# Performance work log

Measured on AMD Instinct MI355X. Metric: run time of the kernel, lower is better.

Reference implementation:

```python
import jax, jax.numpy as jnp
import numpy as np

# irreps: 256x0e + 128x1o + 64x2e  -> feature dim 256 + 384 + 320 = 960
M0, M1, M2 = 256, 128, 64
LOG2 = float(np.log(2.0))

# e3nn normalize2mom constant for shifted-softplus: 1/sqrt(E_{z~N(0,1)}[ssp(z)^2])
_z = np.linspace(-10.0, 10.0, 200001)
_phi = np.exp(-0.5 * _z ** 2) / np.sqrt(2.0 * np.pi)
_f = np.logaddexp(0.0, _z) - LOG2
C_SSP = float(1.0 / np.sqrt(np.trapz(_f ** 2 * _phi, _z)))


def _ssp(x):
    # shifted softplus, normalized to unit second moment as in e3nn Activation
    return C_SSP * (jax.nn.softplus(x) - LOG2)


def setup_inputs() -> dict:
    key = jax.random.key(0)
    ks = jax.random.split(key, 7)
    n = 65536
    return {
        "x": jax.random.normal(ks[0], (n, M0 + 3 * M1 + 5 * M2), dtype=jnp.float32),
        # linear1: l=0 block maps 256x0e -> (256 scalars + 192 gates)x0e
        "w1_s": jax.random.normal(ks[1], (M0, M0 + M1 + M2), dtype=jnp.float32),
        "w1_v1": jax.random.normal(ks[2], (M1, M1), dtype=jnp.float32),
        "w1_v2": jax.random.normal(ks[3], (M2, M2), dtype=jnp.float32),
        # linear2: gate.irreps_out -> irreps_in
        "w2_s": jax.random.normal(ks[4], (M0, M0), dtype=jnp.float32),
        "w2_v1": jax.random.normal(ks[5], (M1, M1), dtype=jnp.float32),
        "w2_v2": jax.random.normal(ks[6], (M2, M2), dtype=jnp.float32),
    }


def reference(x, w1_s, w1_v1, w1_v2, w2_s, w2_v1, w2_v2):
    n = x.shape[0]
    # split input into irrep segments
    x0 = x[:, :M0]                                  # [n, 256] scalars (0e)
    x1 = x[:, M0:M0 + 3 * M1].reshape(n, M1, 3)     # [n, 128, 3] (1o)
    x2 = x[:, M0 + 3 * M1:].reshape(n, M2, 5)       # [n, 64, 5]  (2e)

    # linear1 (per-l block matmuls, e3nn 1/sqrt(fan_in) normalization, no bias)
    s = (x0 @ w1_s) * (1.0 / np.sqrt(M0))                   # [n, 448]
    v1 = jnp.einsum('nic,io->noc', x1, w1_v1) * (1.0 / np.sqrt(M1))
    v2 = jnp.einsum('nic,io->noc', x2, w1_v2) * (1.0 / np.sqrt(M2))

    # Gate: activate scalars, activate gates, multiply gated irreps by gates
    scalars = _ssp(s[:, :M0])          # [n, 256]
    gates = _ssp(s[:, M0:])            # [n, 192] = 128 (for 1o) + 64 (for 2e)
    v1 = v1 * gates[:, :M1, None]
    v2 = v2 * gates[:, M1:, None]

    # linear2
    y0 = (scalars @ w2_s) * (1.0 / np.sqrt(M0))
    y1 = jnp.einsum('nic,io->noc', v1, w2_v1) * (1.0 / np.sqrt(M1))
    y2 = jnp.einsum('nic,io->noc', v2, w2_v2) * (1.0 / np.sqrt(M2))

    y = jnp.concatenate([y0, y1.reshape(n, -1), y2.reshape(n, -1)], axis=1)
    return x + y  # resnet
```

## Files before the change

kernel.cpp:

```cpp
#include <hip/hip_runtime.h>
#include <math.h>

#define XP 960
typedef __attribute__((ext_vector_type(8))) short short8;
typedef __attribute__((ext_vector_type(4))) float f32x4;
typedef __attribute__((ext_vector_type(4))) float fv4;
typedef __attribute__((ext_vector_type(4))) unsigned uint4v;

__device__ short g_pack[221184];

__device__ __forceinline__ short f2bf(float f) {
    union { float f; unsigned u; } v; v.f = f;
    unsigned r = (v.u + 0x7fffu + ((v.u >> 16) & 1u)) >> 16;
    return (short)r;
}
__device__ __forceinline__ unsigned pk2(float a, float b) {
    union { float f; unsigned u; } x, y; x.f = a; y.f = b;
    return ((x.u + 0x8000u) >> 16) | ((y.u + 0x8000u) & 0xffff0000u);
}
__device__ __forceinline__ short8 mk8(unsigned d0, unsigned d1, unsigned d2, unsigned d3) {
    union { uint4v u; short8 s; } cv;
    cv.u = (uint4v){d0, d1, d2, d3};
    return cv.s;
}
__device__ __forceinline__ float ssp(float v, float c) {
    float t = exp2f(fabsf(v) * -1.44269504088896340736f);
    float sp = fmaxf(v, 0.f) + 0.69314718055994530942f * __log2f(1.0f + t);
    return c * (sp - 0.69314718055994530942f);
}

#define WSYNC() asm volatile("s_waitcnt lgkmcnt(0)" ::: "memory")
#define MFMA(a, b, c) __builtin_amdgcn_mfma_f32_16x16x32_bf16((a), (b), (c), 0, 0, 0)
#define NTL(p) __builtin_nontemporal_load((const fv4*)(p))
#define STS(p, v) (*(fv4*)(p) = (v))

__global__ void pack_weights(const float* __restrict__ w1s, const float* __restrict__ w1v1,
                             const float* __restrict__ w1v2, const float* __restrict__ w2s,
                             const float* __restrict__ w2v1, const float* __restrict__ w2v2) {
    int g = blockIdx.x * blockDim.x + threadIdx.x;
    const float* src; int NT, N, dstoff, lg;
    if      (g < 14336) { src = w1s;  NT = 28; N = 448; dstoff = 0;      lg = g; }
    else if (g < 16384) { src = w1v1; NT = 8;  N = 128; dstoff = 114688; lg = g - 14336; }
    else if (g < 16896) { src = w1v2; NT = 4;  N = 64;  dstoff = 131072; lg = g - 16384; }
    else if (g < 25088) { src = w2s;  NT = 16; N = 256; dstoff = 135168; lg = g - 16896; }
    else if (g < 27136) { src = w2v1; NT = 8;  N = 128; dstoff = 200704; lg = g - 25088; }
    else if (g < 27648) { src = w2v2; NT = 4;  N = 64;  dstoff = 217088; lg = g - 27136; }
    else return;
    int lane = lg & 63;
    int t = lg >> 6;
    int nt = t % NT;
    int kt = t / NT;
    int k0 = kt * 32 + (lane >> 4) * 8;
    int n  = nt * 16 + (lane & 15);
    short* dst = g_pack + dstoff + (size_t)lg * 8;
#pragma unroll
    for (int j = 0; j < 8; j++) dst[j] = f2bf(src[(size_t)(k0 + j) * N + n]);
}

__global__ __launch_bounds__(256, 4) void fused_kernel(const float* __restrict__ x,
                                                       float* __restrict__ out,
                                                       float c_ssp) {
    __shared__ __align__(16) short arena[4][16 * 264];

    const int lane = threadIdx.x & 63;
    const int wave = threadIdx.x >> 6;
    const int q = lane >> 4, l15 = lane & 15;
    const int row0 = blockIdx.x * 64 + wave * 16;
    short* S = arena[wave];
    unsigned* Sd = (unsigned*)S;
    const int dwb = l15 * 132 + q * 2;
    const short* Sr = S + l15 * 264 + q * 8;

    const short8* pw1s  = (const short8*)(g_pack + 0);
    const short8* pw1v1 = (const short8*)(g_pack + 114688);
    const short8* pw1v2 = (const short8*)(g_pack + 131072);
    const short8* pw2s  = (const short8*)(g_pack + 135168);
    const short8* pw2v1 = (const short8*)(g_pack + 200704);
    const short8* pw2v2 = (const short8*)(g_pack + 217088);

    const float* xrow = x + (size_t)(row0 + l15) * XP;
    float* yrow = out + (size_t)(row0 + l15) * XP;

    const float S1  = 0.0625f;
    const float SV1 = 0.08838834764831845f;
    const float SV2 = 0.125f;

    short8 xf0[8];
#pragma unroll
    for (int kt = 0; kt < 8; kt++) {
        fv4 u0 = *(const fv4*)(xrow + kt * 32 + q * 8);
        fv4 u1 = *(const fv4*)(xrow + kt * 32 + q * 8 + 4);
        xf0[kt] = mk8(pk2(u0[0], u0[1]), pk2(u0[2], u0[3]), pk2(u1[0], u1[1]), pk2(u1[2], u1[3]));
    }

#pragma unroll 1
    for (int tp = 0; tp < 8; tp++) {
        f32x4 a0 = {0.f,0.f,0.f,0.f}, a1 = {0.f,0.f,0.f,0.f};
#pragma unroll
        for (int kt = 0; kt < 8; kt++) {
            a0 = MFMA(pw1s[(kt * 28 + 2 * tp + 0) * 64 + lane], xf0[kt], a0);
            a1 = MFMA(pw1s[(kt * 28 + 2 * tp + 1) * 64 + lane], xf0[kt], a1);
        }
#pragma unroll
        for (int h = 0; h < 2; h++) {
            f32x4 a = h ? a1 : a0;
            int t = 2 * tp + h;
            Sd[dwb + t * 8]     = pk2(ssp(a[0] * S1, c_ssp), ssp(a[1] * S1, c_ssp));
            Sd[dwb + t * 8 + 1] = pk2(ssp(a[2] * S1, c_ssp), ssp(a[3] * S1, c_ssp));
        }
    }
    f32x4 gacc[12];
#pragma unroll
    for (int tp = 0; tp < 6; tp++) {
        f32x4 a0 = {0.f,0.f,0.f,0.f}, a1 = {0.f,0.f,0.f,0.f};
#pragma unroll
        for (int kt = 0; kt < 8; kt++) {
            a0 = MFMA(pw1s[(kt * 28 + 16 + 2 * tp + 0) * 64 + lane], xf0[kt], a0);
            a1 = MFMA(pw1s[(kt * 28 + 16 + 2 * tp + 1) * 64 + lane], xf0[kt], a1);
        }
        gacc[2 * tp]     = (f32x4){ssp(a0[0]*S1,c_ssp), ssp(a0[1]*S1,c_ssp), ssp(a0[2]*S1,c_ssp), ssp(a0[3]*S1,c_ssp)};
        gacc[2 * tp + 1] = (f32x4){ssp(a1[0]*S1,c_ssp), ssp(a1[1]*S1,c_ssp), ssp(a1[2]*S1,c_ssp), ssp(a1[3]*S1,c_ssp)};
    }
    WSYNC();

    short8 sf[8];
#pragma unroll
    for (int kt = 0; kt < 8; kt++) sf[kt] = *(const short8*)(Sr + kt * 32);
    WSYNC();
#pragma unroll 1
    for (int tp = 0; tp < 8; tp++) {
        f32x4 a0 = {0.f,0.f,0.f,0.f}, a1 = {0.f,0.f,0.f,0.f};
#pragma unroll
        for (int kt = 0; kt < 8; kt++) {
            a0 = MFMA(pw2s[(kt * 16 + 2 * tp + 0) * 64 + lane], sf[kt], a0);
            a1 = MFMA(pw2s[(kt * 16 + 2 * tp + 1) * 64 + lane], sf[kt], a1);
        }
#pragma unroll
        for (int h = 0; h < 2; h++) {
            f32x4 a = h ? a1 : a0;
            int col = (2 * tp + h) * 16 + q * 4;
            fv4 r = NTL(xrow + col);
            fv4 o = {r[0] + a[0] * S1, r[1] + a[1] * S1, r[2] + a[2] * S1, r[3] + a[3] * S1};
            STS(yrow + col, o);
        }
    }

    short8 xf1[3][4];
#pragma unroll
    for (int kt = 0; kt < 4; kt++) {
        float b[24];
        const float* p = xrow + 256 + 3 * (kt * 32 + q * 8);
#pragma unroll
        for (int i = 0; i < 6; i++) *(fv4*)(b + 4 * i) = *(const fv4*)(p + 4 * i);
#pragma unroll
        for (int c = 0; c < 3; c++)
            xf1[c][kt] = mk8(pk2(b[c], b[c+3]), pk2(b[c+6], b[c+9]),
                             pk2(b[c+12], b[c+15]), pk2(b[c+18], b[c+21]));
    }
    short8 vf[3][4];
#pragma unroll
    for (int c = 0; c < 3; c++) {
#pragma unroll
        for (int tp = 0; tp < 4; tp++) {
            f32x4 a0 = {0.f,0.f,0.f,0.f}, a1 = {0.f,0.f,0.f,0.f};
#pragma unroll
            for (int kt = 0; kt < 4; kt++) {
                a0 = MFMA(pw1v1[(kt * 8 + 2 * tp + 0) * 64 + lane], xf1[c][kt], a0);
                a1 = MFMA(pw1v1[(kt * 8 + 2 * tp + 1) * 64 + lane], xf1[c][kt], a1);
            }
#pragma unroll
            for (int h = 0; h < 2; h++) {
                f32x4 a = h ? a1 : a0;
                int t = 2 * tp + h;
                f32x4 g = gacc[t];
                Sd[dwb + t * 8]     = pk2(a[0]*SV1*g[0], a[1]*SV1*g[1]);
                Sd[dwb + t * 8 + 1] = pk2(a[2]*SV1*g[2], a[3]*SV1*g[3]);
            }
        }
        WSYNC();
#pragma unroll
        for (int kt = 0; kt < 4; kt++)
            vf[c][kt] = *(const short8*)(Sr + kt * 32);
        WSYNC();
    }
#pragma unroll 1
    for (int t = 0; t < 8; t++) {
        f32x4 ac0 = {0.f,0.f,0.f,0.f}, ac1 = {0.f,0.f,0.f,0.f}, ac2 = {0.f,0.f,0.f,0.f};
#pragma unroll
        for (int kt = 0; kt < 4; kt++) {
            short8 w = pw2v1[(kt * 8 + t) * 64 + lane];
            ac0 = MFMA(w, vf[0][kt], ac0);
            ac1 = MFMA(w, vf[1][kt], ac1);
            ac2 = MFMA(w, vf[2][kt], ac2);
        }
        int base = 256 + 3 * (t * 16 + q * 4);
        fv4 r0 = NTL(xrow + base), r1 = NTL(xrow + base + 4), r2 = NTL(xrow + base + 8);
        fv4 o0 = {r0[0]+ac0[0]*SV1, r0[1]+ac1[0]*SV1, r0[2]+ac2[0]*SV1, r0[3]+ac0[1]*SV1};
        fv4 o1 = {r1[0]+ac1[1]*SV1, r1[1]+ac2[1]*SV1, r1[2]+ac0[2]*SV1, r1[3]+ac1[2]*SV1};
        fv4 o2 = {r2[0]+ac2[2]*SV1, r2[1]+ac0[3]*SV1, r2[2]+ac1[3]*SV1, r2[3]+ac2[3]*SV1};
        STS(yrow + base, o0); STS(yrow + base + 4, o1); STS(yrow + base + 8, o2);
    }

    short8 xf2[5][2];
#pragma unroll
    for (int kt = 0; kt < 2; kt++) {
        float b[40];
        const float* p = xrow + 640 + 5 * (kt * 32 + q * 8);
#pragma unroll
        for (int i = 0; i < 10; i++) *(fv4*)(b + 4 * i) = *(const fv4*)(p + 4 * i);
#pragma unroll
        for (int c = 0; c < 5; c++)
            xf2[c][kt] = mk8(pk2(b[c], b[c+5]), pk2(b[c+10], b[c+15]),
                             pk2(b[c+20], b[c+25]), pk2(b[c+30], b[c+35]));
    }
    short8 vf2[5][2];
#pragma unroll
    for (int c = 0; c < 5; c++) {
#pragma unroll
        for (int tp = 0; tp < 2; tp++) {
            f32x4 a0 = {0.f,0.f,0.f,0.f}, a1 = {0.f,0.f,0.f,0.f};
#pragma unroll
            for (int kt = 0; kt < 2; kt++) {
                a0 = MFMA(pw1v2[(kt * 4 + 2 * tp + 0) * 64 + lane], xf2[c][kt], a0);
                a1 = MFMA(pw1v2[(kt * 4 + 2 * tp + 1) * 64 + lane], xf2[c][kt], a1);
            }
#pragma unroll
            for (int h = 0; h < 2; h++) {
                f32x4 a = h ? a1 : a0;
                int t = 2 * tp + h;
                f32x4 g = gacc[8 + t];
                Sd[dwb + t * 8]     = pk2(a[0]*SV2*g[0], a[1]*SV2*g[1]);
                Sd[dwb + t * 8 + 1] = pk2(a[2]*SV2*g[2], a[3]*SV2*g[3]);
            }
        }
        WSYNC();
#pragma unroll
        for (int kt = 0; kt < 2; kt++)
            vf2[c][kt] = *(const short8*)(Sr + kt * 32);
        WSYNC();
    }
#pragma unroll 1
    for (int t = 0; t < 4; t++) {
        f32x4 b0 = {0.f,0.f,0.f,0.f}, b1 = {0.f,0.f,0.f,0.f}, b2 = {0.f,0.f,0.f,0.f},
              b3 = {0.f,0.f,0.f,0.f}, b4 = {0.f,0.f,0.f,0.f};
#pragma unroll
        for (int kt = 0; kt < 2; kt++) {
            short8 w = pw2v2[(kt * 4 + t) * 64 + lane];
            b0 = MFMA(w, vf2[0][kt], b0);
            b1 = MFMA(w, vf2[1][kt], b1);
            b2 = MFMA(w, vf2[2][kt], b2);
            b3 = MFMA(w, vf2[3][kt], b3);
            b4 = MFMA(w, vf2[4][kt], b4);
        }
        int base = 640 + 5 * (t * 16 + q * 4);
        fv4 r0 = NTL(xrow + base),      r1 = NTL(xrow + base + 4),
            r2 = NTL(xrow + base + 8),  r3 = NTL(xrow + base + 12),
            r4 = NTL(xrow + base + 16);
        fv4 o0 = {r0[0]+b0[0]*SV2, r0[1]+b1[0]*SV2, r0[2]+b2[0]*SV2, r0[3]+b3[0]*SV2};
        fv4 o1 = {r1[0]+b4[0]*SV2, r1[1]+b0[1]*SV2, r1[2]+b1[1]*SV2, r1[3]+b2[1]*SV2};
        fv4 o2 = {r2[0]+b3[1]*SV2, r2[1]+b4[1]*SV2, r2[2]+b0[2]*SV2, r2[3]+b1[2]*SV2};
        fv4 o3 = {r3[0]+b2[2]*SV2, r3[1]+b3[2]*SV2, r3[2]+b4[2]*SV2, r3[3]+b0[3]*SV2};
        fv4 o4 = {r4[0]+b1[3]*SV2, r4[1]+b2[3]*SV2, r4[2]+b3[3]*SV2, r4[3]+b4[3]*SV2};
        STS(yrow + base, o0); STS(yrow + base + 4, o1); STS(yrow + base + 8, o2);
        STS(yrow + base + 12, o3); STS(yrow + base + 16, o4);
    }
}

static float compute_cssp() {
    const int N = 200001;
    const double dz = 20.0 / 200000.0;
    double sum = 0.0;
    for (int i = 0; i < N; i++) {
        double z = -10.0 + dz * i;
        double f = (z > 0 ? z : 0.0) + log1p(exp(-fabs(z))) - 0.69314718055994530942;
        double phi = exp(-0.5 * z * z) * 0.39894228040143267794;
        double y = f * f * phi;
        sum += (i == 0 || i == N - 1) ? 0.5 * y : y;
    }
    return (float)(1.0 / sqrt(sum * dz));
}

extern "C" void kernel_launch(void* const* d_in, const int* in_sizes, int n_in,
                              void* d_out, int out_size, void* d_ws, size_t ws_size,
                              hipStream_t stream) {
    const float* x    = (const float*)d_in[0];
    const float* w1s  = (const float*)d_in[1];
    const float* w1v1 = (const float*)d_in[2];
    const float* w1v2 = (const float*)d_in[3];
    const float* w2s  = (const float*)d_in[4];
    const float* w2v1 = (const float*)d_in[5];
    const float* w2v2 = (const float*)d_in[6];
    float* out = (float*)d_out;

    static const float c_ssp = compute_cssp();

    int rows = in_sizes[0] / XP;
    int blocks = rows / 64;

    pack_weights<<<108, 256, 0, stream>>>(w1s, w1v1, w1v2, w2s, w2v1, w2v2);
    fused_kernel<<<blocks, 256, 0, stream>>>(x, out, c_ssp);
}
```

Baseline: 631.8 us.

## Process two 16-row tiles per wave to reuse weight fragments across MFMAs

Each wave now handles 32 rows (two 16-row tiles A and B), so every weight fragment loaded from global memory feeds two MFMAs, halving weight traffic per row. The LDS staging buffer is resized to an unpadded 256-wide layout with an XOR swizzle to avoid bank conflicts. Gate activations are kept packed as bf16 pairs to save registers. Launch bounds drop to 2 blocks per CU and the grid halves, which increases register pressure and reduces occupancy and latency hiding.

```diff
diff --git a/kernel.cpp b/kernel.cpp
--- a/kernel.cpp
+++ b/kernel.cpp
@@ -22,6 +22,12 @@
     union { uint4v u; short8 s; } cv;
     cv.u = (uint4v){d0, d1, d2, d3};
     return cv.s;
+}
+__device__ __forceinline__ float bflo(unsigned d) {
+    union { unsigned u; float f; } v; v.u = d << 16; return v.f;
+}
+__device__ __forceinline__ float bfhi(unsigned d) {
+    union { unsigned u; float f; } v; v.u = d & 0xffff0000u; return v.f;
 }
 __device__ __forceinline__ float ssp(float v, float c) {
     float t = exp2f(fabsf(v) * -1.44269504088896340736f);
@@ -57,19 +63,24 @@
     for (int j = 0; j < 8; j++) dst[j] = f2bf(src[(size_t)(k0 + j) * N + n]);
 }
 
-__global__ __launch_bounds__(256, 4) void fused_kernel(const float* __restrict__ x,
+__global__ __launch_bounds__(256, 2) void fused_kernel(const float* __restrict__ x,
                                                        float* __restrict__ out,
                                                        float c_ssp) {
-    __shared__ __align__(16) short arena[4][16 * 264];
+    __shared__ __align__(16) short arena[4][32 * 256];
 
     const int lane = threadIdx.x & 63;
     const int wave = threadIdx.x >> 6;
     const int q = lane >> 4, l15 = lane & 15;
-    const int row0 = blockIdx.x * 64 + wave * 16;
+    const int row0 = blockIdx.x * 128 + wave * 32;
     short* S = arena[wave];
     unsigned* Sd = (unsigned*)S;
-    const int dwb = l15 * 132 + q * 2;
-    const short* Sr = S + l15 * 264 + q * 8;
+
+    const unsigned swzd = (unsigned)((l15 & 7) << 2);
+    const int wlinA = l15 * 128 + q * 2;
+    const int wlinB = wlinA + 2048;
+    const int rlinA = l15 * 512 + q * 16;
+    const int rlinB = rlinA + 8192;
+#define LDSR(linbyte) (*(const short8*)((const char*)S + (((unsigned)(linbyte)) ^ (swzd << 2))))
 
     const short8* pw1s  = (const short8*)(g_pack + 0);
     const short8* pw1v1 = (const short8*)(g_pack + 114688);
@@ -78,192 +89,297 @@
     const short8* pw2v1 = (const short8*)(g_pack + 200704);
     const short8* pw2v2 = (const short8*)(g_pack + 217088);
 
-    const float* xrow = x + (size_t)(row0 + l15) * XP;
-    float* yrow = out + (size_t)(row0 + l15) * XP;
+    const float* xrowA = x + (size_t)(row0 + l15) * XP;
+    const float* xrowB = xrowA + (size_t)16 * XP;
+    float* yrowA = out + (size_t)(row0 + l15) * XP;
+    float* yrowB = yrowA + (size_t)16 * XP;
 
     const float S1  = 0.0625f;
     const float SV1 = 0.08838834764831845f;
     const float SV2 = 0.125f;
 
-    short8 xf0[8];
+    short8 xfA[8], xfB[8];
 #pragma unroll
     for (int kt = 0; kt < 8; kt++) {
-        fv4 u0 = *(const fv4*)(xrow + kt * 32 + q * 8);
-        fv4 u1 = *(const fv4*)(xrow + kt * 32 + q * 8 + 4);
-        xf0[kt] = mk8(pk2(u0[0], u0[1]), pk2(u0[2], u0[3]), pk2(u1[0], u1[1]), pk2(u1[2], u1[3]));
+        fv4 a0 = *(const fv4*)(xrowA + kt * 32 + q * 8);
+        fv4 a1 = *(const fv4*)(xrowA + kt * 32 + q * 8 + 4);
+        fv4 b0 = *(const fv4*)(xrowB + kt * 32 + q * 8);
+        fv4 b1 = *(const fv4*)(xrowB + kt * 32 + q * 8 + 4);
+        xfA[kt] = mk8(pk2(a0[0], a0[1]), pk2(a0[2], a0[3]), pk2(a1[0], a1[1]), pk2(a1[2], a1[3]));
+        xfB[kt] = mk8(pk2(b0[0], b0[1]), pk2(b0[2], b0[3]), pk2(b1[0], b1[1]), pk2(b1[2], b1[3]));
     }
 
 #pragma unroll 1
     for (int tp = 0; tp < 8; tp++) {
-        f32x4 a0 = {0.f,0.f,0.f,0.f}, a1 = {0.f,0.f,0.f,0.f};
+        f32x4 a0A = {0.f,0.f,0.f,0.f}, a1A = {0.f,0.f,0.f,0.f};
+        f32x4 a0B = {0.f,0.f,0.f,0.f}, a1B = {0.f,0.f,0.f,0.f};
 #pragma unroll
         for (int kt = 0; kt < 8; kt++) {
-            a0 = MFMA(pw1s[(kt * 28 + 2 * tp + 0) * 64 + lane], xf0[kt], a0);
-            a1 = MFMA(pw1s[(kt * 28 + 2 * tp + 1) * 64 + lane], xf0[kt], a1);
+            short8 w0 = pw1s[(kt * 28 + 2 * tp + 0) * 64 + lane];
+            short8 w1 = pw1s[(kt * 28 + 2 * tp + 1) * 64 + lane];
+            a0A = MFMA(w0, xfA[kt], a0A);
+            a0B = MFMA(w0, xfB[kt], a0B);
+            a1A = MFMA(w1, xfA[kt], a1A);
+            a1B = MFMA(w1, xfB[kt], a1B);
         }
 #pragma unroll
         for (int h = 0; h < 2; h++) {
-            f32x4 a = h ? a1 : a0;
+            f32x4 aA = h ? a1A : a0A, aB = h ? a1B : a0B;
             int t = 2 * tp + h;
-            Sd[dwb + t * 8]     = pk2(ssp(a[0] * S1, c_ssp), ssp(a[1] * S1, c_ssp));
-            Sd[dwb + t * 8 + 1] = pk2(ssp(a[2] * S1, c_ssp), ssp(a[3] * S1, c_ssp));
-        }
-    }
-    f32x4 gacc[12];
+            { unsigned i = ((unsigned)(wlinA + t * 8)) ^ swzd;
+              Sd[i]     = pk2(ssp(aA[0] * S1, c_ssp), ssp(aA[1] * S1, c_ssp));
+              Sd[i + 1] = pk2(ssp(aA[2] * S1, c_ssp), ssp(aA[3] * S1, c_ssp)); }
+            { unsigned i = ((unsigned)(wlinB + t * 8)) ^ swzd;
+              Sd[i]     = pk2(ssp(aB[0] * S1, c_ssp), ssp(aB[1] * S1, c_ssp));
+              Sd[i + 1] = pk2(ssp(aB[2] * S1, c_ssp), ssp(aB[3] * S1, c_ssp)); }
+        }
+    }
+    unsigned gpkA[24], gpkB[24];
 #pragma unroll
     for (int tp = 0; tp < 6; tp++) {
-        f32x4 a0 = {0.f,0.f,0.f,0.f}, a1 = {0.f,0.f,0.f,0.f};
+        f32x4 a0A = {0.f,0.f,0.f,0.f}, a1A = {0.f,0.f,0.f,0.f};
+        f32x4 a0B = {0.f,0.f,0.f,0.f}, a1B = {0.f,0.f,0.f,0.f};
 #pragma unroll
         for (int kt = 0; kt < 8; kt++) {
-            a0 = MFMA(pw1s[(kt * 28 + 16 + 2 * tp + 0) * 64 + lane], xf0[kt], a0);
-            a1 = MFMA(pw1s[(kt * 28 + 16 + 2 * tp + 1) * 64 + lane], xf0[kt], a1);
-        }
-        gacc[2 * tp]     = (f32x4){ssp(a0[0]*S1,c_ssp), ssp(a0[1]*S1,c_ssp), ssp(a0[2]*S1,c_ssp), ssp(a0[3]*S1,c_ssp)};
-        gacc[2 * tp + 1] = (f32x4){ssp(a1[0]*S1,c_ssp), ssp(a1[1]*S1,c_ssp), ssp(a1[2]*S1,c_ssp), ssp(a1[3]*S1,c_ssp)};
+            short8 w0 = pw1s[(kt * 28 + 16 + 2 * tp + 0) * 64 + lane];
+            short8 w1 = pw1s[(kt * 28 + 16 + 2 * tp + 1) * 64 + lane];
+            a0A = MFMA(w0, xfA[kt], a0A);
+            a0B = MFMA(w0, xfB[kt], a0B);
+            a1A = MFMA(w1, xfA[kt], a1A);
+            a1B = MFMA(w1, xfB[kt], a1B);
+        }
+        gpkA[4*tp+0] = pk2(ssp(a0A[0]*S1,c_ssp), ssp(a0A[1]*S1,c_ssp));
+        gpkA[4*tp+1] = pk2(ssp(a0A[2]*S1,c_ssp), ssp(a0A[3]*S1,c_ssp));
+        gpkA[4*tp+2] = pk2(ssp(a1A[0]*S1,c_ssp), ssp(a1A[1]*S1,c_ssp));
+        gpkA[4*tp+3] = pk2(ssp(a1A[2]*S1,c_ssp), ssp(a1A[3]*S1,c_ssp));
+        gpkB[4*tp+0] = pk2(ssp(a0B[0]*S1,c_ssp), ssp(a0B[1]*S1,c_ssp));
+        gpkB[4*tp+1] = pk2(ssp(a0B[2]*S1,c_ssp), ssp(a0B[3]*S1,c_ssp));
+        gpkB[4*tp+2] = pk2(ssp(a1B[0]*S1,c_ssp), ssp(a1B[1]*S1,c_ssp));
+        gpkB[4*tp+3] = pk2(ssp(a1B[2]*S1,c_ssp), ssp(a1B[3]*S1,c_ssp));
     }
     WSYNC();
 
-    short8 sf[8];
-#pragma unroll
-    for (int kt = 0; kt < 8; kt++) sf[kt] = *(const short8*)(Sr + kt * 32);
+    short8 sfA[8], sfB[8];
+#pragma unroll
+    for (int kt = 0; kt < 8; kt++) {
+        sfA[kt] = LDSR(rlinA + kt * 64);
+        sfB[kt] = LDSR(rlinB + kt * 64);
+    }
     WSYNC();
 #pragma unroll 1
     for (int tp = 0; tp < 8; tp++) {
-        f32x4 a0 = {0.f,0.f,0.f,0.f}, a1 = {0.f,0.f,0.f,0.f};
+        f32x4 a0A = {0.f,0.f,0.f,0.f}, a1A = {0.f,0.f,0.f,0.f};
+        f32x4 a0B = {0.f,0.f,0.f,0.f}, a1B = {0.f,0.f,0.f,0.f};
 #pragma unroll
         for (int kt = 0; kt < 8; kt++) {
-            a0 = MFMA(pw2s[(kt * 16 + 2 * tp + 0) * 64 + lane], sf[kt], a0);
-            a1 = MFMA(pw2s[(kt * 16 + 2 * tp + 1) * 64 + lane], sf[kt], a1);
+            short8 w0 = pw2s[(kt * 16 + 2 * tp + 0) * 64 + lane];
+            short8 w1 = pw2s[(kt * 16 + 2 * tp + 1) * 64 + lane];
+            a0A = MFMA(w0, sfA[kt], a0A);
+            a0B = MFMA(w0, sfB[kt], a0B);
+            a1A = MFMA(w1, sfA[kt], a1A);
+            a1B = MFMA(w1, sfB[kt], a1B);
         }
 #pragma unroll
         for (int h = 0; h < 2; h++) {
-            f32x4 a = h ? a1 : a0;
+            f32x4 aA = h ? a1A : a0A, aB = h ? a1B : a0B;
             int col = (2 * tp + h) * 16 + q * 4;
-            fv4 r = NTL(xrow + col);
-            fv4 o = {r[0] + a[0] * S1, r[1] + a[1] * S1, r[2] + a[2] * S1, r[3] + a[3] * S1};
-            STS(yrow + col, o);
-        }
-    }
-
-    short8 xf1[3][4];
+            fv4 rA = NTL(xrowA + col);
+            fv4 oA = {rA[0] + aA[0]*S1, rA[1] + aA[1]*S1, rA[2] + aA[2]*S1, rA[3] + aA[3]*S1};
+            STS(yrowA + col, oA);
+            fv4 rB = NTL(xrowB + col);
+            fv4 oB = {rB[0] + aB[0]*S1, rB[1] + aB[1]*S1, rB[2] + aB[2]*S1, rB[3] + aB[3]*S1};
+            STS(yrowB + col, oB);
+        }
+    }
+
+    short8 xf1A[3][4], xf1B[3][4];
 #pragma unroll
     for (int kt = 0; kt < 4; kt++) {
-        float b[24];
-        const float* p = xrow + 256 + 3 * (kt * 32 + q * 8);
-#pragma unroll
-        for (int i = 0; i < 6; i++) *(fv4*)(b + 4 * i) = *(const fv4*)(p + 4 * i);
-#pragma unroll
-        for (int c = 0; c < 3; c++)
-            xf1[c][kt] = mk8(pk2(b[c], b[c+3]), pk2(b[c+6], b[c+9]),
-                             pk2(b[c+12], b[c+15]), pk2(b[c+18], b[c+21]));
-    }
-    short8 vf[3][4];
+        float bA[24], bB[24];
+        const float* pA = xrowA + 256 + 3 * (kt * 32 + q * 8);
+        const float* pB = xrowB + 256 + 3 * (kt * 32 + q * 8);
+#pragma unroll
+        for (int i = 0; i < 6; i++) {
+            *(fv4*)(bA + 4 * i) = *(const fv4*)(pA + 4 * i);
+            *(fv4*)(bB + 4 * i) = *(const fv4*)(pB + 4 * i);
+        }
+#pragma unroll
+        for (int c = 0; c < 3; c++) {
+            xf1A[c][kt] = mk8(pk2(bA[c], bA[c+3]), pk2(bA[c+6], bA[c+9]),
+                              pk2(bA[c+12], bA[c+15]), pk2(bA[c+18], bA[c+21]));
+            xf1B[c][kt] = mk8(pk2(bB[c], bB[c+3]), pk2(bB[c+6], bB[c+9]),
+                              pk2(bB[c+12], bB[c+15]), pk2(bB[c+18], bB[c+21]));
+        }
+    }
+    short8 vfA[3][4], vfB[3][4];
 #pragma unroll
     for (int c = 0; c < 3; c++) {
 #pragma unroll
         for (int tp = 0; tp < 4; tp++) {
-            f32x4 a0 = {0.f,0.f,0.f,0.f}, a1 = {0.f,0.f,0.f,0.f};
+            f32x4 a0A = {0.f,0.f,0.f,0.f}, a1A = {0.f,0.f,0.f,0.f};
+            f32x4 a0B = {0.f,0.f,0.f,0.f}, a1B = {0.f,0.f,0.f,0.f};
 #pragma unroll
             for (int kt = 0; kt < 4; kt++) {
-                a0 = MFMA(pw1v1[(kt * 8 + 2 * tp + 0) * 64 + lane], xf1[c][kt], a0);
-                a1 = MFMA(pw1v1[(kt * 8 + 2 * tp + 1) * 64 + lane], xf1[c][kt], a1);
+                short8 w0 = pw1v1[(kt * 8 + 2 * tp + 0) * 64 + lane];
+                short8 w1 = pw1v1[(kt * 8 + 2 * tp + 1) * 64 + lane];
+                a0A = MFMA(w0, xf1A[c][kt], a0A);
+                a0B = MFMA(w0, xf1B[c][kt], a0B);
+                a1A = MFMA(w1, xf1A[c][kt], a1A);
+                a1B = MFMA(w1, xf1B[c][kt], a1B);
             }
 #pragma unroll
             for (int h = 0; h < 2; h++) {
-                f32x4 a = h ? a1 : a0;
+                f32x4 aA = h ? a1A : a0A, aB = h ? a1B : a0B;
                 int t = 2 * tp + h;
-                f32x4 g = gacc[t];
-                Sd[dwb + t * 8]     = pk2(a[0]*SV1*g[0], a[1]*SV1*g[1]);
-                Sd[dwb + t * 8 + 1] = pk2(a[2]*SV1*g[2], a[3]*SV1*g[3]);
+                { unsigned i = ((unsigned)(wlinA + t * 8)) ^ swzd;
+                  Sd[i]     = pk2(aA[0]*SV1*bflo(gpkA[2*t]),   aA[1]*SV1*bfhi(gpkA[2*t]));
+                  Sd[i + 1] = pk2(aA[2]*SV1*bflo(gpkA[2*t+1]), aA[3]*SV1*bfhi(gpkA[2*t+1])); }
+                { unsigned i = ((unsigned)(wlinB + t * 8)) ^ swzd;
+                  Sd[i]     = pk2(aB[0]*SV1*bflo(gpkB[2*t]),   aB[1]*SV1*bfhi(gpkB[2*t]));
+                  Sd[i + 1] = pk2(aB[2]*SV1*bflo(gpkB[2*t+1]), aB[3]*SV1*bfhi(gpkB[2*t+1])); }
             }
         }
         WSYNC();
 #pragma unroll
-        for (int kt = 0; kt < 4; kt++)
-            vf[c][kt] = *(const short8*)(Sr + kt * 32);
+        for (int kt = 0; kt < 4; kt++) {
+            vfA[c][kt] = LDSR(rlinA + kt * 64);
+            vfB[c][kt] = LDSR(rlinB + kt * 64);
+        }
         WSYNC();
     }
 #pragma unroll 1
     for (int t = 0; t < 8; t++) {
-        f32x4 ac0 = {0.f,0.f,0.f,0.f}, ac1 = {0.f,0.f,0.f,0.f}, ac2 = {0.f,0.f,0.f,0.f};
+        f32x4 c0A={0.f,0.f,0.f,0.f}, c1A={0.f,0.f,0.f,0.f}, c2A={0.f,0.f,0.f,0.f};
+        f32x4 c0B={0.f,0.f,0.f,0.f}, c1B={0.f,0.f,0.f,0.f}, c2B={0.f,0.f,0.f,0.f};
 #pragma unroll
         for (int kt = 0; kt < 4; kt++) {
             short8 w = pw2v1[(kt * 8 + t) * 64 + lane];
-            ac0 = MFMA(w, vf[0][kt], ac0);
-            ac1 = MFMA(w, vf[1][kt], ac1);
-            ac2 = MFMA(w, vf[2][kt], ac2);
+            c0A = MFMA(w, vfA[0][kt], c0A);
+            c1A = MFMA(w, vfA[1][kt], c1A);
+            c2A = MFMA(w, vfA[2][kt], c2A);
+            c0B = MFMA(w, vfB[0][kt], c0B);
+            c1B = MFMA(w, vfB[1][kt], c1B);
+            c2B = MFMA(w, vfB[2][kt], c2B);
         }
         int base = 256 + 3 * (t * 16 + q * 4);
-        fv4 r0 = NTL(xrow + base), r1 = NTL(xrow + base + 4), r2 = NTL(xrow + base + 8);
-        fv4 o0 = {r0[0]+ac0[0]*SV1, r0[1]+ac1[0]*SV1, r0[2]+ac2[0]*SV1, r0[3]+ac0[1]*SV1};
-        fv4 o1 = {r1[0]+ac1[1]*SV1, r1[1]+ac2[1]*SV1, r1[2]+ac0[2]*SV1, r1[3]+ac1[2]*SV1};
-        fv4 o2 = {r2[0]+ac2[2]*SV1, r2[1]+ac0[3]*SV1, r2[2]+ac1[3]*SV1, r2[3]+ac2[3]*SV1};
-        STS(yrow + base, o0); STS(yrow + base + 4, o1); STS(yrow + base + 8, o2);
-    }
-
-    short8 xf2[5][2];
+        {
+            fv4 r0 = NTL(xrowA + base), r1 = NTL(xrowA + base + 4), r2 = NTL(xrowA + base + 8);
+            fv4 o0 = {r0[0]+c0A[0]*SV1, r0[1]+c1A[0]*SV1, r0[2]+c2A[0]*SV1, r0[3]+c0A[1]*SV1};
+            fv4 o1 = {r1[0]+c1A[1]*SV1, r1[1]+c2A[1]*SV1, r1[2]+c0A[2]*SV1, r1[3]+c1A[2]*SV1};
+            fv4 o2 = {r2[0]+c2A[2]*SV1, r2[1]+c0A[3]*SV1, r2[2]+c1A[3]*SV1, r2[3]+c2A[3]*SV1};
+            STS(yrowA + base, o0); STS(yrowA + base + 4, o1); STS(yrowA + base + 8, o2);
+        }
+        {
+            fv4 r0 = NTL(xrowB + base), r1 = NTL(xrowB + base + 4), r2 = NTL(xrowB + base + 8);
+            fv4 o0 = {r0[0]+c0B[0]*SV1, r0[1]+c1B[0]*SV1, r0[2]+c2B[0]*SV1, r0[3]+c0B[1]*SV1};
+            fv4 o1 = {r1[0]+c1B[1]*SV1, r1[1]+c2B[1]*SV1, r1[2]+c0B[2]*SV1, r1[3]+c1B[2]*SV1};
+            fv4 o2 = {r2[0]+c2B[2]*SV1, r2[1]+c0B[3]*SV1, r2[2]+c1B[3]*SV1, r2[3]+c2B[3]*SV1};
+            STS(yrowB + base, o0); STS(yrowB + base + 4, o1); STS(yrowB + base + 8, o2);
+        }
+    }
+
+    short8 xf2A[5][2], xf2B[5][2];
 #pragma unroll
     for (int kt = 0; kt < 2; kt++) {
-        float b[40];
-        const float* p = xrow + 640 + 5 * (kt * 32 + q * 8);
-#pragma unroll
-        for (int i = 0; i < 10; i++) *(fv4*)(b + 4 * i) = *(const fv4*)(p + 4 * i);
-#pragma unroll
-        for (int c = 0; c < 5; c++)
-            xf2[c][kt] = mk8(pk2(b[c], b[c+5]), pk2(b[c+10], b[c+15]),
-                             pk2(b[c+20], b[c+25]), pk2(b[c+30], b[c+35]));
-    }
-    short8 vf2[5][2];
+        float bA[40], bB[40];
+        const float* pA = xrowA + 640 + 5 * (kt * 32 + q * 8);
+        const float* pB = xrowB + 640 + 5 * (kt * 32 + q * 8);
+#pragma unroll
+        for (int i = 0; i < 10; i++) {
+            *(fv4*)(bA + 4 * i) = *(const fv4*)(pA + 4 * i);
+            *(fv4*)(bB + 4 * i) = *(const fv4*)(pB + 4 * i);
+        }
+#pragma unroll
+        for (int c = 0; c < 5; c++) {
+            xf2A[c][kt] = mk8(pk2(bA[c], bA[c+5]), pk2(bA[c+10], bA[c+15]),
+                              pk2(bA[c+20], bA[c+25]), pk2(bA[c+30], bA[c+35]));
+            xf2B[c][kt] = mk8(pk2(bB[c], bB[c+5]), pk2(bB[c+10], bB[c+15]),
+                              pk2(bB[c+20], bB[c+25]), pk2(bB[c+30], bB[c+35]));
+        }
+    }
+    short8 vf2A[5][2], vf2B[5][2];
 #pragma unroll
     for (int c = 0; c < 5; c++) {
 #pragma unroll
         for (int tp = 0; tp < 2; tp++) {
-            f32x4 a0 = {0.f,0.f,0.f,0.f}, a1 = {0.f,0.f,0.f,0.f};
+            f32x4 a0A = {0.f,0.f,0.f,0.f}, a1A = {0.f,0.f,0.f,0.f};
+            f32x4 a0B = {0.f,0.f,0.f,0.f}, a1B = {0.f,0.f,0.f,0.f};
 #pragma unroll
             for (int kt = 0; kt < 2; kt++) {
-                a0 = MFMA(pw1v2[(kt * 4 + 2 * tp + 0) * 64 + lane], xf2[c][kt], a0);
-                a1 = MFMA(pw1v2[(kt * 4 + 2 * tp + 1) * 64 + lane], xf2[c][kt], a1);
+                short8 w0 = pw1v2[(kt * 4 + 2 * tp + 0) * 64 + lane];
+                short8 w1 = pw1v2[(kt * 4 + 2 * tp + 1) * 64 + lane];
+                a0A = MFMA(w0, xf2A[c][kt], a0A);
+                a0B = MFMA(w0, xf2B[c][kt], a0B);
+                a1A = MFMA(w1, xf2A[c][kt], a1A);
+                a1B = MFMA(w1, xf2B[c][kt], a1B);
             }
 #pragma unroll
             for (int h = 0; h < 2; h++) {
-                f32x4 a = h ? a1 : a0;
+                f32x4 aA = h ? a1A : a0A, aB = h ? a1B : a0B;
                 int t = 2 * tp + h;
-                f32x4 g = gacc[8 + t];
-                Sd[dwb + t * 8]     = pk2(a[0]*SV2*g[0], a[1]*SV2*g[1]);
-                Sd[dwb + t * 8 + 1] = pk2(a[2]*SV2*g[2], a[3]*SV2*g[3]);
+                { unsigned i = ((unsigned)(wlinA + t * 8)) ^ swzd;
+                  Sd[i]     = pk2(aA[0]*SV2*bflo(gpkA[16+2*t]),   aA[1]*SV2*bfhi(gpkA[16+2*t]));
+                  Sd[i + 1] = pk2(aA[2]*SV2*bflo(gpkA[16+2*t+1]), aA[3]*SV2*bfhi(gpkA[16+2*t+1])); }
+                { unsigned i = ((unsigned)(wlinB + t * 8)) ^ swzd;
+                  Sd[i]     = pk2(aB[0]*SV2*bflo(gpkB[16+2*t]),   aB[1]*SV2*bfhi(gpkB[16+2*t]));
+                  Sd[i + 1] = pk2(aB[2]*SV2*bflo(gpkB[16+2*t+1]), aB[3]*SV2*bfhi(gpkB[16+2*t+1])); }
             }
         }
         WSYNC();
 #pragma unroll
-        for (int kt = 0; kt < 2; kt++)
-            vf2[c][kt] = *(const short8*)(Sr + kt * 32);
+        for (int kt = 0; kt < 2; kt++) {
+            vf2A[c][kt] = LDSR(rlinA + kt * 64);
+            vf2B[c][kt] = LDSR(rlinB + kt * 64);
+        }
         WSYNC();
     }
 #pragma unroll 1
     for (int t = 0; t < 4; t++) {
-        f32x4 b0 = {0.f,0.f,0.f,0.f}, b1 = {0.f,0.f,0.f,0.f}, b2 = {0.f,0.f,0.f,0.f},
-              b3 = {0.f,0.f,0.f,0.f}, b4 = {0.f,0.f,0.f,0.f};
+        f32x4 b0A={0.f,0.f,0.f,0.f}, b1A={0.f,0.f,0.f,0.f}, b2A={0.f,0.f,0.f,0.f},
+              b3A={0.f,0.f,0.f,0.f}, b4A={0.f,0.f,0.f,0.f};
+        f32x4 b0B={0.f,0.f,0.f,0.f}, b1B={0.f,0.f,0.f,0.f}, b2B={0.f,0.f,0.f,0.f},
+              b3B={0.f,0.f,0.f,0.f}, b4B={0.f,0.f,0.f,0.f};
 #pragma unroll
         for (int kt = 0; kt < 2; kt++) {
             short8 w = pw2v2[(kt * 4 + t) * 64 + lane];
-            b0 = MFMA(w, vf2[0][kt], b0);
-            b1 = MFMA(w, vf2[1][kt], b1);
-            b2 = MFMA(w, vf2[2][kt], b2);
-            b3 = MFMA(w, vf2[3][kt], b3);
-            b4 = MFMA(w, vf2[4][kt], b4);
+            b0A = MFMA(w, vf2A[0][kt], b0A);
+            b1A = MFMA(w, vf2A[1][kt], b1A);
+            b2A = MFMA(w, vf2A[2][kt], b2A);
+            b3A = MFMA(w, vf2A[3][kt], b3A);
+            b4A = MFMA(w, vf2A[4][kt], b4A);
+            b0B = MFMA(w, vf2B[0][kt], b0B);
+            b1B = MFMA(w, vf2B[1][kt], b1B);
+            b2B = MFMA(w, vf2B[2][kt], b2B);
+            b3B = MFMA(w, vf2B[3][kt], b3B);
+            b4B = MFMA(w, vf2B[4][kt], b4B);
         }
         int base = 640 + 5 * (t * 16 + q * 4);
-        fv4 r0 = NTL(xrow + base),      r1 = NTL(xrow + base + 4),
-            r2 = NTL(xrow + base + 8),  r3 = NTL(xrow + base + 12),
-            r4 = NTL(xrow + base + 16);
-        fv4 o0 = {r0[0]+b0[0]*SV2, r0[1]+b1[0]*SV2, r0[2]+b2[0]*SV2, r0[3]+b3[0]*SV2};
-        fv4 o1 = {r1[0]+b4[0]*SV2, r1[1]+b0[1]*SV2, r1[2]+b1[1]*SV2, r1[3]+b2[1]*SV2};
-        fv4 o2 = {r2[0]+b3[1]*SV2, r2[1]+b4[1]*SV2, r2[2]+b0[2]*SV2, r2[3]+b1[2]*SV2};
-        fv4 o3 = {r3[0]+b2[2]*SV2, r3[1]+b3[2]*SV2, r3[2]+b4[2]*SV2, r3[3]+b0[3]*SV2};
-        fv4 o4 = {r4[0]+b1[3]*SV2, r4[1]+b2[3]*SV2, r4[2]+b3[3]*SV2, r4[3]+b4[3]*SV2};
-        STS(yrow + base, o0); STS(yrow + base + 4, o1); STS(yrow + base + 8, o2);
-        STS(yrow + base + 12, o3); STS(yrow + base + 16, o4);
-    }
+        {
+            fv4 r0 = NTL(xrowA + base),      r1 = NTL(xrowA + base + 4),
+                r2 = NTL(xrowA + base + 8),  r3 = NTL(xrowA + base + 12),
+                r4 = NTL(xrowA + base + 16);
+            fv4 o0 = {r0[0]+b0A[0]*SV2, r0[1]+b1A[0]*SV2, r0[2]+b2A[0]*SV2, r0[3]+b3A[0]*SV2};
+            fv4 o1 = {r1[0]+b4A[0]*SV2, r1[1]+b0A[1]*SV2, r1[2]+b1A[1]*SV2, r1[3]+b2A[1]*SV2};
+            fv4 o2 = {r2[0]+b3A[1]*SV2, r2[1]+b4A[1]*SV2, r2[2]+b0A[2]*SV2, r2[3]+b1A[2]*SV2};
+            fv4 o3 = {r3[0]+b2A[2]*SV2, r3[1]+b3A[2]*SV2, r3[2]+b4A[2]*SV2, r3[3]+b0A[3]*SV2};
+            fv4 o4 = {r4[0]+b1A[3]*SV2, r4[1]+b2A[3]*SV2, r4[2]+b3A[3]*SV2, r4[3]+b4A[3]*SV2};
+            STS(yrowA + base, o0); STS(yrowA + base + 4, o1); STS(yrowA + base + 8, o2);
+            STS(yrowA + base + 12, o3); STS(yrowA + base + 16, o4);
+        }
+        {
+            fv4 r0 = NTL(xrowB + base),      r1 = NTL(xrowB + base + 4),
+                r2 = NTL(xrowB + base + 8),  r3 = NTL(xrowB + base + 12),
+                r4 = NTL(xrowB + base + 16);
+            fv4 o0 = {r0[0]+b0B[0]*SV2, r0[1]+b1B[0]*SV2, r0[2]+b2B[0]*SV2, r0[3]+b3B[0]*SV2};
+            fv4 o1 = {r1[0]+b4B[0]*SV2, r1[1]+b0B[1]*SV2, r1[2]+b1B[1]*SV2, r1[3]+b2B[1]*SV2};
+            fv4 o2 = {r2[0]+b3B[1]*SV2, r2[1]+b4B[1]*SV2, r2[2]+b0B[2]*SV2, r2[3]+b1B[2]*SV2};
+            fv4 o3 = {r3[0]+b2B[2]*SV2, r3[1]+b3B[2]*SV2, r3[2]+b4B[2]*SV2, r3[3]+b0B[3]*SV2};
+            fv4 o4 = {r4[0]+b1B[3]*SV2, r4[1]+b2B[3]*SV2, r4[2]+b3B[3]*SV2, r4[3]+b4B[3]*SV2};
+            STS(yrowB + base, o0); STS(yrowB + base + 4, o1); STS(yrowB + base + 8, o2);
+            STS(yrowB + base + 12, o3); STS(yrowB + base + 16, o4);
+        }
+    }
+#undef LDSR
 }
 
 static float compute_cssp() {
@@ -295,7 +411,7 @@
     static const float c_ssp = compute_cssp();
 
     int rows = in_sizes[0] / XP;
-    int blocks = rows / 64;
+    int blocks = rows / 128;
 
     pack_weights<<<108, 256, 0, stream>>>(w1s, w1v1, w1v2, w2s, w2v1, w2v2);
     fused_kernel<<<blocks, 256, 0, stream>>>(x, out, c_ssp);
```

Measured after the change: 615.5 us. -2.6%, faster.
